# Optimization experiments

Hardware: AMD Instinct MI355X
Metric: run time of the kernel (lower is better)

Reference implementation:

```python
import jax, jax.numpy as jnp
import numpy as np
import math

HEADS = 2
DH = 64
INNER = HEADS * DH  # 128
TOPK = 128
ALPHA = 10.0
N_FREQ = 8  # feature_dim // (2*input_dim) = 64 // 8
OMEGAS = jnp.logspace(1.0, math.log10(128.0), N_FREQ)           # sigma_q = 128
OMEGAS_L = [jnp.logspace(1.0, math.log10(s), N_FREQ) for s in (128.0, 32.0)]
LAYER_NUM = 2


def calc_gamma(grid, omegas):
    # grid: (Q, 4) -> (Q, 4*2*n_freq)
    arg = jnp.pi * grid[:, :, None] * omegas[None, None, :]      # (Q,4,n)
    g = jnp.concatenate([jnp.sin(arg), jnp.cos(arg)], axis=-1)   # (Q,4,2n)
    return g.reshape(grid.shape[0], -1)


def setup_inputs() -> dict:
    key = jax.random.key(0)
    ks = jax.random.split(key, 20)
    B, Q, L, HD, FD, OD = 2, 4096, 1024, 256, 64, 1

    def w(k, shape, fan_in):
        return jax.random.normal(k, shape, dtype=jnp.float32) * (1.0 / np.sqrt(fan_in))

    inp = {
        'x': jax.random.uniform(ks[0], (B, Q, 4), dtype=jnp.float32),
        'tokens': jax.random.normal(ks[1], (B, L, HD), dtype=jnp.float32),
        'query_W': w(ks[2], (FD, HD), FD),
        'query_b': jnp.zeros((HD,), jnp.float32),
        'q_W': w(ks[3], (HD, INNER), HD),
        'kv_W': w(ks[4], (HD, 2 * INNER), HD),
        'out_W': w(ks[5], (INNER, HD), INNER),
        'out_b': jnp.zeros((HD,), jnp.float32),
        'band_W': w(ks[6], (LAYER_NUM, FD, HD), FD),
        'band_b': jnp.zeros((LAYER_NUM, HD), jnp.float32),
        'mod_W': w(ks[7], (LAYER_NUM, HD, HD), HD),
        'mod_b': jnp.zeros((LAYER_NUM, HD), jnp.float32),
        'hv_W': w(ks[8], (LAYER_NUM - 1, HD, HD), HD),
        'hv_b': jnp.zeros((LAYER_NUM - 1, HD), jnp.float32),
        'outl_W': w(ks[9], (LAYER_NUM, HD, OD), HD),
        'outl_b': jnp.zeros((LAYER_NUM, OD), jnp.float32),
        'gD': 8, 'gH': 8, 'gW': 8, 'gT': 8,
    }
    return inp


def reference(x, tokens, query_W, query_b, q_W, kv_W, out_W, out_b,
              band_W, band_b, mod_W, mod_b, hv_W, hv_b, outl_W, outl_b,
              gD, gH, gW, gT):
    B, Q, _ = x.shape
    L = tokens.shape[1]
    grid = x[0]  # (Q, 4) — torch code uses x[0] for all batches

    # --- patch index + approximate relative distances -> sparse attn indices ---
    z_i = (grid[:, 0] * gD).astype(jnp.int32)
    y_i = (grid[:, 1] * gH).astype(jnp.int32)
    x_i = (grid[:, 2] * gW).astype(jnp.int32)
    t_i = (grid[:, 3] * gT).astype(jnp.int32)
    idx = ((t_i * gD + z_i) * gH + y_i) * gW + x_i               # (Q,)
    N = gD * gH * gW * gT
    t = idx / N                                                  # (Q,) float
    tok_pos = (jnp.arange(L, dtype=jnp.float32) + 0.5) / L       # (L,)
    bias = ALPHA * (t[:, None] - tok_pos[None, :]) ** 2          # (Q, L)
    # top-k SMALLEST distances (identical across batch, compute once)
    _, attn_idx = jax.lax.top_k(-bias, TOPK)                     # (Q, k)

    # --- query features ---
    gamma_q = calc_gamma(grid, OMEGAS)                           # (Q, 64)
    x_q = jax.nn.relu(gamma_q @ query_W + query_b)               # (Q, 256)
    x_q = jnp.broadcast_to(x_q[None], (B, Q, x_q.shape[-1]))

    # --- sparse shared-token cross attention ---
    scale = DH ** -0.5
    q = (x_q @ q_W).reshape(B, Q, HEADS, DH)                     # (B,Q,H,Dh)
    kv = tokens @ kv_W                                           # (B,L,2*inner)
    k_full, v_full = kv[..., :INNER], kv[..., INNER:]            # (B,L,inner)
    k_sp = k_full[:, attn_idx, :].reshape(B, Q, TOPK, HEADS, DH)  # (B,Q,k,H,Dh)
    v_sp = v_full[:, attn_idx, :].reshape(B, Q, TOPK, HEADS, DH)
    sim = jnp.einsum('bqhd,bqkhd->bhqk', q, k_sp) * scale        # (B,H,Q,k)
    attn = jax.nn.softmax(sim, axis=-1)
    o = jnp.einsum('bhqk,bqkhd->bqhd', attn, v_sp).reshape(B, Q, INNER)
    modulation = o @ out_W + out_b                               # (B,Q,256)

    # --- per-band modulation ---
    mods = []
    for l in range(LAYER_NUM):
        gamma_l = calc_gamma(grid, OMEGAS_L[l])                  # (Q, 64)
        h_l = jax.nn.relu(gamma_l @ band_W[l] + band_b[l])       # (Q, 256)
        m_l = jax.nn.relu(h_l[None] + modulation @ mod_W[l] + mod_b[l])
        mods.append(m_l)

    h_v = [mods[0]]
    for i in range(LAYER_NUM - 1):
        h_v.append(jax.nn.relu((mods[i + 1] + h_v[i]) @ hv_W[i] + hv_b[i]))

    out = sum(h_v[i] @ outl_W[i] + outl_b[i] for i in range(LAYER_NUM))
    return out  # (B, Q, output_dim)
```

## Files before the change

kernel.cpp:

```cpp
#include <hip/hip_runtime.h>
#include <math.h>

#define BN     2
#define QN     4096
#define LN     1024
#define TOPKN  128
#define PI_F   3.14159265358979323846f

#define K_OM0  0.3642064529893673
#define K_OM1  0.1661644014008115

#define NCMAX  320
#define PFP    328

typedef __attribute__((ext_vector_type(8))) short  s16x8;
typedef __attribute__((ext_vector_type(4))) short  s16x4;
typedef __attribute__((ext_vector_type(4))) float  f32x4;
typedef unsigned short u16;

__device__ __forceinline__ u16 f2bf(float f) {
    unsigned int u = __float_as_uint(f);
    u = (u + 0x7FFFu + ((u >> 16) & 1u)) >> 16;
    return (u16)u;
}

__device__ __forceinline__ size_t wtile(int n, int k, int K) {
    return (size_t)((n >> 4) * (K >> 5) + (k >> 5)) * 512 + (n & 15) * 32 + (k & 31);
}
__device__ __forceinline__ size_t kidx(int b, int l, int d) {
    return (((size_t)(b * 64 + (l >> 4)) * 16 + (d >> 3)) * 16 + (l & 15)) * 8 + (d & 7);
}
__device__ __forceinline__ size_t vidx(int b, int n, int k) {
    return (((size_t)(b * 8 + (n >> 4)) * 128 + (k >> 3)) * 16 + (n & 15)) * 8 + (k & 7);
}

struct KvS { u16 tok[32 * 264]; u16 stage[256 * 40]; float vtile[128][40]; };
struct QS  { float shx[128]; u16 gam[32 * 72]; u16 xq[32 * 264]; u16 stage[256 * 40]; };
struct TrS { float tile[32][33]; };
struct SoS { int hist[1024]; int cur[1024]; };
union PrepS { KvS kv; QS q; TrS tr; SoS so; };

__global__ __launch_bounds__(1024) void prep_kernel(
    const float* __restrict__ tokens, const float* __restrict__ kv_W,
    const float* __restrict__ x, const float* __restrict__ query_W,
    const float* __restrict__ query_b, const float* __restrict__ q_W,
    const float* __restrict__ outW, const float* __restrict__ bandW,
    const float* __restrict__ modW, const float* __restrict__ hvW,
    const int* __restrict__ gDp, const int* __restrict__ gHp,
    const int* __restrict__ gWp, const int* __restrict__ gTp,
    float* __restrict__ qall, u16* __restrict__ kbf, u16* __restrict__ vtbf,
    u16* __restrict__ outT, u16* __restrict__ bandT,
    u16* __restrict__ modT, u16* __restrict__ hvT,
    int* __restrict__ perm, int* __restrict__ ssort)
{
    __shared__ __align__(16) PrepS sm;
    const int bid = blockIdx.x;
    const int t   = threadIdx.x;
    const int wid = t >> 6, lane = t & 63;
    const int quad = lane >> 4, l16 = lane & 15;

    if (bid < 64) {
        int l0 = bid * 32;
        int b = l0 >> 10, lloc = l0 & 1023;
        #pragma unroll
        for (int i = 0; i < 8; i++) {
            int idx = i * 1024 + t; int row = idx >> 8, col = idx & 255;
            sm.kv.tok[row * 264 + col] = f2bf(tokens[(size_t)(l0 + row) * 256 + col]);
        }
        int m0 = (wid & 1) * 16;
        int c0 = (wid >> 1) * 32;
        f32x4 acc[2];
        acc[0] = (f32x4){0.f, 0.f, 0.f, 0.f};
        acc[1] = (f32x4){0.f, 0.f, 0.f, 0.f};
        for (int kc = 0; kc < 8; kc++) {
            __syncthreads();
            #pragma unroll
            for (int i = 0; i < 8; i++) {
                int idx = i * 1024 + t; int k = idx >> 8, n = idx & 255;
                sm.kv.stage[n * 40 + k] = f2bf(kv_W[(size_t)(kc * 32 + k) * 256 + n]);
            }
            __syncthreads();
            s16x8 a = *(const s16x8*)&sm.kv.tok[(m0 + l16) * 264 + kc * 32 + quad * 8];
            #pragma unroll
            for (int sub = 0; sub < 2; sub++) {
                s16x8 bfr = *(const s16x8*)&sm.kv.stage[(c0 + sub * 16 + l16) * 40 + quad * 8];
                acc[sub] = __builtin_amdgcn_mfma_f32_16x16x32_bf16(a, bfr, acc[sub], 0, 0, 0);
            }
        }
        #pragma unroll
        for (int sub = 0; sub < 2; sub++) {
            int col = c0 + sub * 16 + l16;
            if (col < 128) {
                #pragma unroll
                for (int r = 0; r < 4; r++) {
                    int lg = l0 + m0 + quad * 4 + r;
                    kbf[kidx(lg >> 10, lg & 1023, col)] = f2bf(acc[sub][r]);
                }
            } else {
                #pragma unroll
                for (int r = 0; r < 4; r++)
                    sm.kv.vtile[col - 128][m0 + quad * 4 + r] = acc[sub][r];
            }
        }
        __syncthreads();
        {
            int col = t >> 3, rg = (t & 7) * 4;
            float4 v4 = *(const float4*)&sm.kv.vtile[col][rg];
            s16x4 pk;
            pk[0] = (short)f2bf(v4.x); pk[1] = (short)f2bf(v4.y);
            pk[2] = (short)f2bf(v4.z); pk[3] = (short)f2bf(v4.w);
            *(s16x4*)&vtbf[vidx(b, col, lloc + rg)] = pk;
        }
    } else if (bid < 192) {
        int p0 = (bid - 64) * 32;
        if (t < 128) sm.q.shx[t] = x[p0 * 4 + t];
        __syncthreads();
        #pragma unroll
        for (int j = 0; j < 2; j++) {
            int e = t * 2 + j;
            int g = e >> 6, f = e & 63;
            int c = f >> 4, jj = f & 15, oi = jj & 7;
            float om = (float)(10.0 * exp((double)oi * K_OM0));
            float arg = PI_F * sm.q.shx[g * 4 + c] * om;
            sm.q.gam[g * 72 + f] = f2bf((jj < 8) ? sinf(arg) : cosf(arg));
        }
        int m0 = (wid & 1) * 16;
        {
            int c0 = (wid >> 1) * 32;
            f32x4 acc[2];
            acc[0] = (f32x4){0.f, 0.f, 0.f, 0.f};
            acc[1] = (f32x4){0.f, 0.f, 0.f, 0.f};
            for (int kc = 0; kc < 2; kc++) {
                __syncthreads();
                #pragma unroll
                for (int i = 0; i < 8; i++) {
                    int idx = i * 1024 + t; int k = idx >> 8, n = idx & 255;
                    sm.q.stage[n * 40 + k] = f2bf(query_W[(size_t)(kc * 32 + k) * 256 + n]);
                }
                __syncthreads();
                s16x8 a = *(const s16x8*)&sm.q.gam[(m0 + l16) * 72 + kc * 32 + quad * 8];
                #pragma unroll
                for (int sub = 0; sub < 2; sub++) {
                    s16x8 bfr = *(const s16x8*)&sm.q.stage[(c0 + sub * 16 + l16) * 40 + quad * 8];
                    acc[sub] = __builtin_amdgcn_mfma_f32_16x16x32_bf16(a, bfr, acc[sub], 0, 0, 0);
                }
            }
            #pragma unroll
            for (int sub = 0; sub < 2; sub++) {
                int col = c0 + sub * 16 + l16;
                float bias = query_b[col];
                #pragma unroll
                for (int r = 0; r < 4; r++)
                    sm.q.xq[(m0 + quad * 4 + r) * 264 + col] = f2bf(fmaxf(acc[sub][r] + bias, 0.f));
            }
        }
        {
            int n0q = (wid >> 1) * 16;
            f32x4 acc2 = (f32x4){0.f, 0.f, 0.f, 0.f};
            for (int kc = 0; kc < 8; kc++) {
                __syncthreads();
                #pragma unroll
                for (int i = 0; i < 4; i++) {
                    int idx = i * 1024 + t; int k = idx >> 7, n = idx & 127;
                    sm.q.stage[n * 40 + k] = f2bf(q_W[(size_t)(kc * 32 + k) * 128 + n]);
                }
                __syncthreads();
                s16x8 a = *(const s16x8*)&sm.q.xq[(m0 + l16) * 264 + kc * 32 + quad * 8];
                s16x8 bfr = *(const s16x8*)&sm.q.stage[(n0q + l16) * 40 + quad * 8];
                acc2 = __builtin_amdgcn_mfma_f32_16x16x32_bf16(a, bfr, acc2, 0, 0, 0);
            }
            #pragma unroll
            for (int r = 0; r < 4; r++)
                qall[(size_t)(p0 + m0 + quad * 4 + r) * 128 + n0q + l16] = acc2[r];
        }
    } else if (bid < 448) {
        int bid2 = bid - 192;
        const float* src; u16* dst; int K, N, lt;
        if      (bid2 < 32)  { src = outW;  dst = outT;  K = 128; N = 256; lt = bid2; }
        else if (bid2 < 64)  { src = bandW; dst = bandT; K = 128; N = 256; lt = bid2 - 32; }
        else if (bid2 < 192) { src = modW;  dst = modT;  K = 512; N = 256; lt = bid2 - 64; }
        else                 { src = hvW;   dst = hvT;   K = 256; N = 256; lt = bid2 - 192; }
        int tk = K >> 5;
        int ktile = lt % tk, nt = lt / tk;
        int k0 = ktile * 32, n0 = nt * 32;
        int tx = t & 31, ty = (t >> 5) & 31;
        sm.tr.tile[ty][tx] = src[(size_t)(k0 + ty) * N + n0 + tx];
        __syncthreads();
        dst[wtile(n0 + ty, k0 + tx, K)] = f2bf(sm.tr.tile[tx][ty]);
    } else {
        int gD = gDp[0], gH = gHp[0], gW = gWp[0], gT = gTp[0];
        int Ng = gD * gH * gW * gT;
        sm.so.hist[t] = 0;
        __syncthreads();
        int sarr[4];
        #pragma unroll
        for (int i = 0; i < 4; i++) {
            int q = i * 1024 + t;
            float4 xv = *(const float4*)&x[q * 4];
            int zi = (int)(xv.x * (float)gD);
            int yi = (int)(xv.y * (float)gH);
            int xi = (int)(xv.z * (float)gW);
            int ti = (int)(xv.w * (float)gT);
            int idx = ((ti * gD + zi) * gH + yi) * gW + xi;
            float tt = (float)idx / (float)Ng;
            int s = (int)ceilf(tt * (float)LN - ((float)(TOPKN / 2) + 0.5f));
            s = min(max(s, 0), LN - TOPKN);
            sarr[i] = s;
            atomicAdd(&sm.so.hist[s], 1);
        }
        __syncthreads();
        int cnt = sm.so.hist[t];
        sm.so.cur[t] = cnt;
        __syncthreads();
        for (int off = 1; off < 1024; off <<= 1) {
            int u = (t >= off) ? sm.so.cur[t - off] : 0;
            __syncthreads();
            sm.so.cur[t] += u;
            __syncthreads();
        }
        int excl = sm.so.cur[t] - cnt;
        __syncthreads();
        sm.so.hist[t] = excl;
        __syncthreads();
        #pragma unroll
        for (int i = 0; i < 4; i++) {
            int q = i * 1024 + t;
            int pos = atomicAdd(&sm.so.hist[sarr[i]], 1);
            perm[pos] = q;
            ssort[pos] = sarr[i];
        }
    }
}

__global__ __launch_bounds__(1024, 8) void fused_kernel(
    const float* __restrict__ x,
    const u16* __restrict__ kbf, const u16* __restrict__ vtbf,
    const float* __restrict__ qall,
    const int* __restrict__ perm, const int* __restrict__ ssort,
    const u16* __restrict__ outT, const float* __restrict__ out_b,
    const u16* __restrict__ bandT, const float* __restrict__ band_b,
    const u16* __restrict__ modT, const float* __restrict__ mod_b,
    const u16* __restrict__ hvT, const float* __restrict__ hv_b,
    const float* __restrict__ outl_W, const float* __restrict__ outl_b,
    float* __restrict__ out)
{
    const int bid = blockIdx.x;
    const int b   = bid >> 8;
    const int sp0 = (bid & 255) * 16;
    const int t   = threadIdx.x;
    const int wid = t >> 6, lane = t & 63;
    const int quad = lane >> 4, l16 = lane & 15;

    __shared__ __align__(16) u16 q_bf[16 * 136];
    __shared__ __align__(16) u16 gam_lds[32 * 72];
    __shared__ __align__(16) float scores32[32 * PFP];
    __shared__ __align__(16) u16 o_lds[16 * 136];
    __shared__ float fin[256];
    __shared__ float sh_xc[64];
    __shared__ int sh_pq[16], sh_s[16];

    u16* modu_lds = (u16*)scores32;
    u16* s01_lds  = ((u16*)scores32) + 16 * 264;

    if (t < 16) { sh_pq[t] = perm[sp0 + t]; sh_s[t] = ssort[sp0 + t]; }
    __syncthreads();

    {
        int m = t >> 6, d = (t & 63) * 2;
        float2 qv = *(const float2*)&qall[(size_t)sh_pq[m] * 128 + d];
        unsigned int pk = (unsigned int)f2bf(qv.x) | ((unsigned int)f2bf(qv.y) << 16);
        *(unsigned int*)&q_bf[m * 136 + d] = pk;
    }
    if (t < 64) sh_xc[t] = x[(size_t)sh_pq[t >> 2] * 4 + (t & 3)];
    __syncthreads();

    #pragma unroll
    for (int j = 0; j < 2; j++) {
        int e = t * 2 + j;
        int l = e >> 10, g = (e >> 6) & 15, f = e & 63;
        int c = f >> 4, jj = f & 15, oi = jj & 7;
        float om = (float)(10.0 * exp((double)oi * (l ? K_OM1 : K_OM0)));
        float arg = PI_F * sh_xc[g * 4 + c] * om;
        gam_lds[(l * 16 + g) * 72 + f] = f2bf((jj < 8) ? sinf(arg) : cosf(arg));
    }

    const int u0    = sh_s[0] & ~15;
    const int ncols = min((sh_s[15] + 128 - u0 + 31) & ~31, NCMAX);
    const int nsub  = ncols >> 4;
    const int nkc   = ncols >> 5;

    {
        s16x8 aq00 = *(const s16x8*)&q_bf[l16 * 136 + quad * 8];
        s16x8 aq01 = *(const s16x8*)&q_bf[l16 * 136 + 32 + quad * 8];
        s16x8 aq10 = *(const s16x8*)&q_bf[l16 * 136 + 64 + quad * 8];
        s16x8 aq11 = *(const s16x8*)&q_bf[l16 * 136 + 96 + quad * 8];
        for (int j = wid; j < 2 * nsub; j += 16) {
            int h = (j >= nsub) ? 1 : 0;
            int sub = j - h * nsub;
            int lrow = u0 + sub * 16 + l16;
            f32x4 acc = (f32x4){0.f, 0.f, 0.f, 0.f};
            s16x8 b0 = *(const s16x8*)&kbf[kidx(b, lrow, h * 64 + quad * 8)];
            s16x8 b1 = *(const s16x8*)&kbf[kidx(b, lrow, h * 64 + 32 + quad * 8)];
            acc = __builtin_amdgcn_mfma_f32_16x16x32_bf16(h ? aq10 : aq00, b0, acc, 0, 0, 0);
            acc = __builtin_amdgcn_mfma_f32_16x16x32_bf16(h ? aq11 : aq01, b1, acc, 0, 0, 0);
            #pragma unroll
            for (int r = 0; r < 4; r++)
                scores32[(h * 16 + quad * 4 + r) * PFP + sub * 16 + l16] = acc[r];
        }
    }
    __syncthreads();

    {
        int g = wid;
        int sg = sh_s[g];
        #pragma unroll
        for (int rr = 0; rr < 2; rr++) {
            int row = g + rr * 16;
            float vals[5]; int ok[5];
            float mx = -1e30f;
            #pragma unroll
            for (int i = 0; i < 5; i++) {
                int c = lane + 64 * i;
                float v = scores32[row * PFP + c] * 0.125f;
                int key = u0 + c;
                int o2 = (c < ncols) && (key >= sg) && (key < sg + 128);
                vals[i] = v; ok[i] = o2;
                if (o2) mx = fmaxf(mx, v);
            }
            #pragma unroll
            for (int off = 1; off < 64; off <<= 1) mx = fmaxf(mx, __shfl_xor(mx, off));
            float sum = 0.f, e5[5];
            #pragma unroll
            for (int i = 0; i < 5; i++) {
                float e = ok[i] ? expf(vals[i] - mx) : 0.f;
                e5[i] = e; sum += e;
            }
            #pragma unroll
            for (int off = 1; off < 64; off <<= 1) sum += __shfl_xor(sum, off);
            float inv = 1.f / sum;
            u16* prow = (u16*)&scores32[row * PFP];
            #pragma unroll
            for (int i = 0; i < 5; i++) {
                int c = lane + 64 * i;
                if (c < ncols) prow[c] = f2bf(e5[i] * inv);
            }
        }
    }
    __syncthreads();

    if (wid < 8) {
        int n0 = wid * 16;
        int hh = n0 >> 6;
        const u16* prow = (const u16*)&scores32[(hh * 16 + l16) * PFP];
        f32x4 acc = (f32x4){0.f, 0.f, 0.f, 0.f};
        for (int kc = 0; kc < nkc; kc++) {
            s16x8 a = *(const s16x8*)&prow[kc * 32 + quad * 8];
            int koff = u0 + kc * 32 + quad * 8;
            koff = min(koff, 1016);
            s16x8 bfr = *(const s16x8*)&vtbf[vidx(b, n0 + l16, koff)];
            acc = __builtin_amdgcn_mfma_f32_16x16x32_bf16(a, bfr, acc, 0, 0, 0);
        }
        #pragma unroll
        for (int r = 0; r < 4; r++)
            o_lds[(quad * 4 + r) * 136 + n0 + l16] = f2bf(acc[r]);
    }
    __syncthreads();

    const int n0 = wid * 16;
    float m0f[4];

    {
        f32x4 acc = (f32x4){0.f, 0.f, 0.f, 0.f};
        #pragma unroll
        for (int kc = 0; kc < 4; kc++) {
            s16x8 a = *(const s16x8*)&o_lds[l16 * 136 + kc * 32 + quad * 8];
            s16x8 bfr = *(const s16x8*)&outT[wtile(n0 + l16, kc * 32 + quad * 8, 128)];
            acc = __builtin_amdgcn_mfma_f32_16x16x32_bf16(a, bfr, acc, 0, 0, 0);
        }
        int col = n0 + l16;
        float bias = out_b[col];
        #pragma unroll
        for (int r = 0; r < 4; r++)
            modu_lds[(quad * 4 + r) * 264 + col] = f2bf(acc[r] + bias);
    }
    __syncthreads();

    #pragma unroll
    for (int l = 0; l < 2; l++) {
        f32x4 acc1 = (f32x4){0.f, 0.f, 0.f, 0.f};
        f32x4 acc2 = (f32x4){0.f, 0.f, 0.f, 0.f};
        #pragma unroll
        for (int kc = 0; kc < 2; kc++) {
            s16x8 a = *(const s16x8*)&gam_lds[(l * 16 + l16) * 72 + kc * 32 + quad * 8];
            s16x8 bfr = *(const s16x8*)&bandT[wtile(n0 + l16, l * 64 + kc * 32 + quad * 8, 128)];
            acc1 = __builtin_amdgcn_mfma_f32_16x16x32_bf16(a, bfr, acc1, 0, 0, 0);
        }
        #pragma unroll
        for (int kc = 0; kc < 8; kc++) {
            s16x8 a = *(const s16x8*)&modu_lds[l16 * 264 + kc * 32 + quad * 8];
            s16x8 bfr = *(const s16x8*)&modT[wtile(n0 + l16, l * 256 + kc * 32 + quad * 8, 512)];
            acc2 = __builtin_amdgcn_mfma_f32_16x16x32_bf16(a, bfr, acc2, 0, 0, 0);
        }
        int col = n0 + l16;
        float bb = band_b[l * 256 + col];
        float mb = mod_b[l * 256 + col];
        #pragma unroll
        for (int r = 0; r < 4; r++) {
            float hval = fmaxf(acc1[r] + bb, 0.f);
            float mval = fmaxf(hval + acc2[r] + mb, 0.f);
            if (l == 0) m0f[r] = mval;
            else s01_lds[(quad * 4 + r) * 264 + col] = f2bf(m0f[r] + mval);
        }
    }
    __syncthreads();

    {
        f32x4 acc = (f32x4){0.f, 0.f, 0.f, 0.f};
        #pragma unroll
        for (int kc = 0; kc < 8; kc++) {
            s16x8 a = *(const s16x8*)&s01_lds[l16 * 264 + kc * 32 + quad * 8];
            s16x8 bfr = *(const s16x8*)&hvT[wtile(n0 + l16, kc * 32 + quad * 8, 256)];
            acc = __builtin_amdgcn_mfma_f32_16x16x32_bf16(a, bfr, acc, 0, 0, 0);
        }
        int col = n0 + l16;
        float w0 = outl_W[col], w1 = outl_W[256 + col], hb = hv_b[col];
        #pragma unroll
        for (int r = 0; r < 4; r++) {
            float hvv = fmaxf(acc[r] + hb, 0.f);
            float pv = m0f[r] * w0 + hvv * w1;
            #pragma unroll
            for (int off = 1; off < 16; off <<= 1) pv += __shfl_xor(pv, off);
            if (l16 == 0) fin[wid * 16 + quad * 4 + r] = pv;
        }
    }
    __syncthreads();
    if (t < 16) {
        float s2 = outl_b[0] + outl_b[1];
        #pragma unroll
        for (int w = 0; w < 16; w++) s2 += fin[w * 16 + t];
        out[(size_t)b * QN + sh_pq[t]] = s2;
    }
}

extern "C" void kernel_launch(void* const* d_in, const int* in_sizes, int n_in,
                              void* d_out, int out_size, void* d_ws, size_t ws_size,
                              hipStream_t stream)
{
    const float* x       = (const float*)d_in[0];
    const float* tokens  = (const float*)d_in[1];
    const float* query_W = (const float*)d_in[2];
    const float* query_b = (const float*)d_in[3];
    const float* q_W     = (const float*)d_in[4];
    const float* kv_W    = (const float*)d_in[5];
    const float* out_W   = (const float*)d_in[6];
    const float* out_b   = (const float*)d_in[7];
    const float* band_W  = (const float*)d_in[8];
    const float* band_b  = (const float*)d_in[9];
    const float* mod_W   = (const float*)d_in[10];
    const float* mod_b   = (const float*)d_in[11];
    const float* hv_W    = (const float*)d_in[12];
    const float* hv_b    = (const float*)d_in[13];
    const float* outl_W  = (const float*)d_in[14];
    const float* outl_b  = (const float*)d_in[15];
    const int*   gD      = (const int*)d_in[16];
    const int*   gH      = (const int*)d_in[17];
    const int*   gW      = (const int*)d_in[18];
    const int*   gT      = (const int*)d_in[19];

    float* ws   = (float*)d_ws;
    float* qall = ws;
    u16* wb = (u16*)(ws + 524288);
    u16* kbf   = wb;
    u16* vtbf  = wb + 262144;
    u16* outT  = wb + 524288;
    u16* bandT = wb + 557056;
    u16* modT  = wb + 589824;
    u16* hvT   = wb + 720896;
    int* perm  = (int*)(wb + 786432);
    int* ssort = perm + 4096;
    float* out = (float*)d_out;

    prep_kernel<<<449, 1024, 0, stream>>>(tokens, kv_W, x, query_W, query_b, q_W,
                                          out_W, band_W, mod_W, hv_W,
                                          gD, gH, gW, gT,
                                          qall, kbf, vtbf, outT, bandT, modT, hvT,
                                          perm, ssort);
    fused_kernel<<<512, 1024, 0, stream>>>(x, kbf, vtbf, qall, perm, ssort,
        outT, out_b, bandT, band_b, modT, mod_b, hvT, hv_b,
        outl_W, outl_b, out);
}
```

Before: 128.7 us.

## Use fast math intrinsics, bf16 q storage, batched weight transposes and wave-shuffle scan

Swaps double-precision exp and precise sin/cos/exp for exp2f and the __sinf/__cosf/__expf intrinsics in the gamma feature and softmax paths. The query projection is stored as bf16 in prep instead of fp32, which halves that workspace traffic and drops the per-element conversion in the fused kernel. Weight-transpose blocks now handle 8 tiles each, cutting the prep grid from 449 to 225 blocks, and the 1024-wide prefix scan uses wave shuffles instead of a barrier-per-step LDS scan. The LDS score padding is also changed. Fast intrinsics lose accuracy for large sin/cos arguments, up to about 128*pi here.

```diff
diff --git a/kernel.cpp b/kernel.cpp
--- a/kernel.cpp
+++ b/kernel.cpp
@@ -7,11 +7,11 @@
 #define TOPKN  128
 #define PI_F   3.14159265358979323846f
 
-#define K_OM0  0.3642064529893673
-#define K_OM1  0.1661644014008115
+#define LOG2R0 0.52543879f
+#define LOG2R1 0.23972456f
 
 #define NCMAX  320
-#define PFP    328
+#define PFP    332
 
 typedef __attribute__((ext_vector_type(8))) short  s16x8;
 typedef __attribute__((ext_vector_type(4))) short  s16x4;
@@ -36,7 +36,7 @@
 
 struct KvS { u16 tok[32 * 264]; u16 stage[256 * 40]; float vtile[128][40]; };
 struct QS  { float shx[128]; u16 gam[32 * 72]; u16 xq[32 * 264]; u16 stage[256 * 40]; };
-struct TrS { float tile[32][33]; };
+struct TrS { float tile[8][32][33]; };
 struct SoS { int hist[1024]; int cur[1024]; };
 union PrepS { KvS kv; QS q; TrS tr; SoS so; };
 
@@ -48,7 +48,7 @@
     const float* __restrict__ modW, const float* __restrict__ hvW,
     const int* __restrict__ gDp, const int* __restrict__ gHp,
     const int* __restrict__ gWp, const int* __restrict__ gTp,
-    float* __restrict__ qall, u16* __restrict__ kbf, u16* __restrict__ vtbf,
+    u16* __restrict__ qall, u16* __restrict__ kbf, u16* __restrict__ vtbf,
     u16* __restrict__ outT, u16* __restrict__ bandT,
     u16* __restrict__ modT, u16* __restrict__ hvT,
     int* __restrict__ perm, int* __restrict__ ssort)
@@ -120,9 +120,9 @@
             int e = t * 2 + j;
             int g = e >> 6, f = e & 63;
             int c = f >> 4, jj = f & 15, oi = jj & 7;
-            float om = (float)(10.0 * exp((double)oi * K_OM0));
+            float om = 10.0f * exp2f((float)oi * LOG2R0);
             float arg = PI_F * sm.q.shx[g * 4 + c] * om;
-            sm.q.gam[g * 72 + f] = f2bf((jj < 8) ? sinf(arg) : cosf(arg));
+            sm.q.gam[g * 72 + f] = f2bf((jj < 8) ? __sinf(arg) : __cosf(arg));
         }
         int m0 = (wid & 1) * 16;
         {
@@ -171,22 +171,36 @@
             }
             #pragma unroll
             for (int r = 0; r < 4; r++)
-                qall[(size_t)(p0 + m0 + quad * 4 + r) * 128 + n0q + l16] = acc2[r];
-        }
-    } else if (bid < 448) {
-        int bid2 = bid - 192;
-        const float* src; u16* dst; int K, N, lt;
-        if      (bid2 < 32)  { src = outW;  dst = outT;  K = 128; N = 256; lt = bid2; }
-        else if (bid2 < 64)  { src = bandW; dst = bandT; K = 128; N = 256; lt = bid2 - 32; }
-        else if (bid2 < 192) { src = modW;  dst = modT;  K = 512; N = 256; lt = bid2 - 64; }
-        else                 { src = hvW;   dst = hvT;   K = 256; N = 256; lt = bid2 - 192; }
-        int tk = K >> 5;
-        int ktile = lt % tk, nt = lt / tk;
-        int k0 = ktile * 32, n0 = nt * 32;
+                qall[(size_t)(p0 + m0 + quad * 4 + r) * 128 + n0q + l16] = f2bf(acc2[r]);
+        }
+    } else if (bid < 224) {
+        int base = (bid - 192) * 8;
         int tx = t & 31, ty = (t >> 5) & 31;
-        sm.tr.tile[ty][tx] = src[(size_t)(k0 + ty) * N + n0 + tx];
-        __syncthreads();
-        dst[wtile(n0 + ty, k0 + tx, K)] = f2bf(sm.tr.tile[tx][ty]);
+        #pragma unroll
+        for (int it = 0; it < 8; it++) {
+            int lt_g = base + it;
+            const float* src; int K, lt;
+            if (lt_g < 32)       { src = outW;  K = 128; lt = lt_g; }
+            else if (lt_g < 64)  { src = bandW; K = 128; lt = lt_g - 32; }
+            else if (lt_g < 192) { src = modW;  K = 512; lt = lt_g - 64; }
+            else                 { src = hvW;   K = 256; lt = lt_g - 192; }
+            int tk = K >> 5;
+            int k0 = (lt % tk) * 32, n0 = (lt / tk) * 32;
+            sm.tr.tile[it][ty][tx] = src[(size_t)(k0 + ty) * 256 + n0 + tx];
+        }
+        __syncthreads();
+        #pragma unroll
+        for (int it = 0; it < 8; it++) {
+            int lt_g = base + it;
+            u16* dst; int K, lt;
+            if (lt_g < 32)       { dst = outT;  K = 128; lt = lt_g; }
+            else if (lt_g < 64)  { dst = bandT; K = 128; lt = lt_g - 32; }
+            else if (lt_g < 192) { dst = modT;  K = 512; lt = lt_g - 64; }
+            else                 { dst = hvT;   K = 256; lt = lt_g - 192; }
+            int tk = K >> 5;
+            int k0 = (lt % tk) * 32, n0 = (lt / tk) * 32;
+            dst[wtile(n0 + ty, k0 + tx, K)] = f2bf(sm.tr.tile[it][tx][ty]);
+        }
     } else {
         int gD = gDp[0], gH = gHp[0], gW = gWp[0], gT = gTp[0];
         int Ng = gD * gH * gW * gT;
@@ -210,17 +224,26 @@
         }
         __syncthreads();
         int cnt = sm.so.hist[t];
-        sm.so.cur[t] = cnt;
-        __syncthreads();
-        for (int off = 1; off < 1024; off <<= 1) {
-            int u = (t >= off) ? sm.so.cur[t - off] : 0;
-            __syncthreads();
-            sm.so.cur[t] += u;
-            __syncthreads();
-        }
-        int excl = sm.so.cur[t] - cnt;
-        __syncthreads();
-        sm.so.hist[t] = excl;
+        int incl = cnt;
+        #pragma unroll
+        for (int off = 1; off < 64; off <<= 1) {
+            int u = __shfl_up(incl, off);
+            if (lane >= off) incl += u;
+        }
+        if (lane == 63) sm.so.cur[wid] = incl;
+        __syncthreads();
+        if (wid == 0) {
+            int v = (lane < 16) ? sm.so.cur[lane] : 0;
+            #pragma unroll
+            for (int off = 1; off < 16; off <<= 1) {
+                int u = __shfl_up(v, off);
+                if (lane >= off) v += u;
+            }
+            if (lane < 16) sm.so.cur[lane] = v;
+        }
+        __syncthreads();
+        int woff = wid ? sm.so.cur[wid - 1] : 0;
+        sm.so.hist[t] = woff + incl - cnt;
         __syncthreads();
         #pragma unroll
         for (int i = 0; i < 4; i++) {
@@ -235,7 +258,7 @@
 __global__ __launch_bounds__(1024, 8) void fused_kernel(
     const float* __restrict__ x,
     const u16* __restrict__ kbf, const u16* __restrict__ vtbf,
-    const float* __restrict__ qall,
+    const u16* __restrict__ qall,
     const int* __restrict__ perm, const int* __restrict__ ssort,
     const u16* __restrict__ outT, const float* __restrict__ out_b,
     const u16* __restrict__ bandT, const float* __restrict__ band_b,
@@ -267,9 +290,8 @@
 
     {
         int m = t >> 6, d = (t & 63) * 2;
-        float2 qv = *(const float2*)&qall[(size_t)sh_pq[m] * 128 + d];
-        unsigned int pk = (unsigned int)f2bf(qv.x) | ((unsigned int)f2bf(qv.y) << 16);
-        *(unsigned int*)&q_bf[m * 136 + d] = pk;
+        *(unsigned int*)&q_bf[m * 136 + d] =
+            *(const unsigned int*)&qall[(size_t)sh_pq[m] * 128 + d];
     }
     if (t < 64) sh_xc[t] = x[(size_t)sh_pq[t >> 2] * 4 + (t & 3)];
     __syncthreads();
@@ -279,9 +301,9 @@
         int e = t * 2 + j;
         int l = e >> 10, g = (e >> 6) & 15, f = e & 63;
         int c = f >> 4, jj = f & 15, oi = jj & 7;
-        float om = (float)(10.0 * exp((double)oi * (l ? K_OM1 : K_OM0)));
+        float om = 10.0f * exp2f((float)oi * (l ? LOG2R1 : LOG2R0));
         float arg = PI_F * sh_xc[g * 4 + c] * om;
-        gam_lds[(l * 16 + g) * 72 + f] = f2bf((jj < 8) ? sinf(arg) : cosf(arg));
+        gam_lds[(l * 16 + g) * 72 + f] = f2bf((jj < 8) ? __sinf(arg) : __cosf(arg));
     }
 
     const int u0    = sh_s[0] & ~15;
@@ -332,7 +354,7 @@
             float sum = 0.f, e5[5];
             #pragma unroll
             for (int i = 0; i < 5; i++) {
-                float e = ok[i] ? expf(vals[i] - mx) : 0.f;
+                float e = ok[i] ? __expf(vals[i] - mx) : 0.f;
                 e5[i] = e; sum += e;
             }
             #pragma unroll
@@ -468,7 +490,7 @@
     const int*   gT      = (const int*)d_in[19];
 
     float* ws   = (float*)d_ws;
-    float* qall = ws;
+    u16* qall   = (u16*)ws;
     u16* wb = (u16*)(ws + 524288);
     u16* kbf   = wb;
     u16* vtbf  = wb + 262144;
@@ -480,7 +502,7 @@
     int* ssort = perm + 4096;
     float* out = (float*)d_out;
 
-    prep_kernel<<<449, 1024, 0, stream>>>(tokens, kv_W, x, query_W, query_b, q_W,
+    prep_kernel<<<225, 1024, 0, stream>>>(tokens, kv_W, x, query_W, query_b, q_W,
                                           out_W, band_W, mod_W, hv_W,
                                           gD, gH, gW, gT,
                                           qall, kbf, vtbf, outT, bandT, modT, hvT,
```

After: 125.8 us. 2.3% less time.
